# Optimization experiments

Measured on AMD Instinct MI355X. Metric: run time of the kernel, lower is better.

## Reference

```python
import jax, jax.numpy as jnp
import numpy as np

T, B, OBS, ACT = 512, 256, 64, 8
H, C = 1024, 512  # h_size, cell_size


def setup_inputs() -> dict:
    key = jax.random.key(0)
    ks = jax.random.split(key, 12)
    u = lambda k, shape, s: jax.random.uniform(k, shape, jnp.float32, -s, s)
    inp = {
        "xs": jax.random.normal(ks[0], (T, B, OBS), jnp.float32),
        "h0": jnp.zeros((B, C), jnp.float32),
        "c0": jnp.zeros((B, C), jnp.float32),
        "h_masks": (jax.random.uniform(ks[1], (T, B, 1)) < 0.05).astype(jnp.float32),
        # input_layer (kaiming-ish uniform fan-in init)
        "W_in": u(ks[2], (H, OBS), 1.0 / np.sqrt(OBS)),
        "b_in": jnp.zeros((H,), jnp.float32),
        # LSTMCell params, PyTorch layout: gates order (i, f, g, o), [4C, in]
        "W_ih": u(ks[3], (4 * C, H), 1.0 / np.sqrt(C)),
        "b_ih": u(ks[4], (4 * C,), 1.0 / np.sqrt(C)),
        "W_hh": u(ks[5], (4 * C, C), 1.0 / np.sqrt(C)),
        "b_hh": u(ks[6], (4 * C,), 1.0 / np.sqrt(C)),
        # mean_layer with mini_weight_init: U(-0.003, 0.003), zero bias
        "W_mean": u(ks[7], (ACT, C), 0.003),
        "b_mean": jnp.zeros((ACT,), jnp.float32),
        "log_std_param": jax.random.normal(ks[8], (ACT,)) * 1e-10 - 1.0,
    }
    return inp


def reference(xs, h0, c0, h_masks, W_in, b_in, W_ih, b_ih, W_hh, b_hh,
              W_mean, b_mean, log_std_param):
    # xs: [T, B, OBS] -> relu embedding [T, B, H]
    x_emb = jax.nn.relu(jnp.einsum('tbo,ho->tbh', xs, W_in) + b_in)
    # Precompute the input-to-gates GEMM for all timesteps at once: [T, B, 4C]
    gx = jnp.einsum('tbh,gh->tbg', x_emb, W_ih) + b_ih

    cell = W_hh.shape[1]

    def step(carry, inp):
        h, c = carry
        g_x, mask = inp                      # g_x: [B,4C], mask: [B,1]
        keep = 1.0 - mask
        h = h * keep
        c = c * keep
        gates = g_x + h @ W_hh.T + b_hh      # [B, 4C]
        i, f, g, o = jnp.split(gates, 4, axis=-1)
        c = jax.nn.sigmoid(f) * c + jax.nn.sigmoid(i) * jnp.tanh(g)
        h = jax.nn.sigmoid(o) * jnp.tanh(c)
        return (h, c), h

    (h_T, c_T), hiddens = jax.lax.scan(step, (h0, c0), (gx, h_masks))
    # hiddens: [T, B, C]
    means = jnp.tanh(jnp.einsum('tbc,ac->tba', hiddens, W_mean) + b_mean)
    log_std = jnp.broadcast_to(log_std_param, means.shape)
    return means, log_std, h_T, c_T
```

## Files before the change

kernel.cpp:

```cpp
#include <hip/hip_runtime.h>
#include <cstdint>
#include <cstddef>

typedef unsigned short ushort_t;
typedef unsigned int uint_t;
typedef __attribute__((ext_vector_type(8))) __bf16 bf16x8;
typedef __attribute__((ext_vector_type(4))) float f32x4;
typedef __attribute__((ext_vector_type(2))) unsigned int u32x2;

static constexpr int T_STEPS = 512;
static constexpr int BATCH   = 256;
static constexpr int OBS_D   = 64;
static constexpr int ACT_D   = 8;
static constexpr int HID_D   = 1024;
static constexpr int CELL_D  = 512;
static constexpr int GATE_D  = 4 * CELL_D;
static constexpr int SCAN_BLOCKS = 256;

__device__ __forceinline__ float bf2f(ushort_t s) {
    uint_t u = ((uint_t)s) << 16;
    float f;
    __builtin_memcpy(&f, &u, 4);
    return f;
}
__device__ __forceinline__ ushort_t f2bf(float x) {
    uint_t u;
    __builtin_memcpy(&u, &x, 4);
    u += 0x7fffu + ((u >> 16) & 1u);
    return (ushort_t)(u >> 16);
}

__device__ __forceinline__ float sigmoid_fast(float x) {
    return __builtin_amdgcn_rcpf(1.f + __expf(-x));
}
__device__ __forceinline__ float tanh_fast(float x) {
    const float e = __expf(-2.f * fabsf(x));
    const float r = (1.f - e) * __builtin_amdgcn_rcpf(1.f + e);
    return copysignf(r, x);
}

__global__ __launch_bounds__(256)
void cvt_f32_bf16(const float* __restrict__ in, ushort_t* __restrict__ out)
{
    const size_t i = ((size_t)blockIdx.x * 256 + threadIdx.x) * 8;
    const float4 v0 = *(const float4*)(in + i);
    const float4 v1 = *(const float4*)(in + i + 4);
    uint4 p;
    p.x = (uint_t)f2bf(v0.x) | ((uint_t)f2bf(v0.y) << 16);
    p.y = (uint_t)f2bf(v0.z) | ((uint_t)f2bf(v0.w) << 16);
    p.z = (uint_t)f2bf(v1.x) | ((uint_t)f2bf(v1.y) << 16);
    p.w = (uint_t)f2bf(v1.z) | ((uint_t)f2bf(v1.w) << 16);
    *(uint4*)(out + i) = p;
}

__global__ __launch_bounds__(256)
void permute_gate_rows(const float* __restrict__ W, ushort_t* __restrict__ Wp, int K)
{
    const int P = blockIdx.x;
    const int c = P >> 2, g = P & 3;
    const float* src = W + (size_t)(g * CELL_D + c) * K;
    ushort_t* dst = Wp + (size_t)P * K;
    for (int k = threadIdx.x; k < K; k += 256) dst[k] = f2bf(src[k]);
}

__global__ __launch_bounds__(256)
void permute_whh_rows(const float* __restrict__ W, ushort_t* __restrict__ Wp, int K)
{
    const int P = blockIdx.x;
    const int blk = P >> 6, rl = P & 63;
    const int t = rl >> 4, qq = (rl >> 2) & 3, r = rl & 3;
    const float* src = W + (size_t)(r * CELL_D + blk * 16 + t * 4 + qq) * K;
    ushort_t* dst = Wp + (size_t)P * K;
    for (int k = threadIdx.x; k < K; k += 256) dst[k] = f2bf(src[k]);
}

__global__ __launch_bounds__(256)
void permute_bias(const float* __restrict__ b, float* __restrict__ bp)
{
    const int P = blockIdx.x * 256 + threadIdx.x;
    bp[P] = b[(P & 3) * CELL_D + (P >> 2)];
}

template<int OUT_MODE>
__global__ __launch_bounds__(256)
void gemm_mfma_nt(const ushort_t* __restrict__ A, const ushort_t* __restrict__ B,
                  const float* __restrict__ bias, void* __restrict__ out_,
                  int N, int K)
{
    __shared__ __align__(16) ushort_t As[128 * 32];
    __shared__ __align__(16) ushort_t Bs[128 * 32];
    const int tid  = threadIdx.x;
    const int lane = tid & 63;
    const int wid  = tid >> 6;
    const int wr   = (wid >> 1) * 64;
    const int wc   = (wid & 1) * 64;
    const int m0 = blockIdx.y * 128;
    const int n0 = blockIdx.x * 128;

    const int srow = tid >> 2;
    const int sv   = tid & 3;
    const int fr   = lane & 15;
    const int fo   = lane >> 4;

    f32x4 acc[4][4];
#pragma unroll
    for (int i = 0; i < 4; ++i)
#pragma unroll
        for (int j = 0; j < 4; ++j) acc[i][j] = (f32x4){0.f, 0.f, 0.f, 0.f};

    const ushort_t* Apt = A + (size_t)(m0 + srow) * K + sv * 8;
    const ushort_t* Bpt = B + (size_t)(n0 + srow) * K + sv * 8;
    uint4* As4 = (uint4*)As;
    uint4* Bs4 = (uint4*)Bs;
    const bf16x8* Af = (const bf16x8*)As;
    const bf16x8* Bf = (const bf16x8*)Bs;

    for (int k0 = 0; k0 < K; k0 += 32) {
        const uint4 a0 = *(const uint4*)(Apt + k0);
        const uint4 a1 = *(const uint4*)(Apt + (size_t)64 * K + k0);
        const uint4 b0 = *(const uint4*)(Bpt + k0);
        const uint4 b1 = *(const uint4*)(Bpt + (size_t)64 * K + k0);
        __syncthreads();
        As4[srow * 4 + sv]        = a0;
        As4[(64 + srow) * 4 + sv] = a1;
        Bs4[srow * 4 + sv]        = b0;
        Bs4[(64 + srow) * 4 + sv] = b1;
        __syncthreads();

        bf16x8 av[4], bv[4];
#pragma unroll
        for (int m = 0; m < 4; ++m) av[m] = Af[(wr + m * 16 + fr) * 4 + fo];
#pragma unroll
        for (int n = 0; n < 4; ++n) bv[n] = Bf[(wc + n * 16 + fr) * 4 + fo];
#pragma unroll
        for (int m = 0; m < 4; ++m)
#pragma unroll
            for (int n = 0; n < 4; ++n)
                acc[m][n] = __builtin_amdgcn_mfma_f32_16x16x32_bf16(
                    av[m], bv[n], acc[m][n], 0, 0, 0);
    }

#pragma unroll
    for (int n = 0; n < 4; ++n) {
        const int col = n0 + wc + n * 16 + fr;
        const float bvv = bias[col];
#pragma unroll
        for (int m = 0; m < 4; ++m) {
            const int row0 = m0 + wr + m * 16 + fo * 4;
#pragma unroll
            for (int r = 0; r < 4; ++r) {
                const float v = acc[m][n][r] + bvv;
                if constexpr (OUT_MODE == 1)
                    ((ushort_t*)out_)[(size_t)(row0 + r) * N + col] = f2bf(fmaxf(v, 0.f));
                else if constexpr (OUT_MODE == 2)
                    ((ushort_t*)out_)[(size_t)(row0 + r) * N + col] = f2bf(v);
                else
                    ((float*)out_)[(size_t)(row0 + r) * N + col] = v;
            }
        }
    }
}

__device__ __forceinline__ void loadq(uint4 (&d0)[4], uint4 (&d1)[4],
                                      const ushort_t* hr0, const ushort_t* hr1,
                                      int base)
{
#pragma unroll
    for (int j = 0; j < 4; ++j) {
        d0[j] = *(const uint4*)(hr0 + (base + j) * 32);
        d1[j] = *(const uint4*)(hr1 + (base + j) * 32);
    }
}

__device__ __forceinline__ void compq(const uint4 (&d0)[4], const uint4 (&d1)[4],
                                      const char* wsrow, int q16, int xmask,
                                      int base, f32x4& acc0, f32x4& acc1)
{
#pragma unroll
    for (int j = 0; j < 4; ++j) {
        bf16x8 hv0, hv1;
        __builtin_memcpy(&hv0, &d0[j], 16);
        __builtin_memcpy(&hv1, &d1[j], 16);
        const int koff = ((base + j) * 64 + q16) ^ xmask;
        const bf16x8 av = *(const bf16x8*)(wsrow + koff);
        acc0 = __builtin_amdgcn_mfma_f32_16x16x32_bf16(av, hv0, acc0, 0, 0, 0);
        acc1 = __builtin_amdgcn_mfma_f32_16x16x32_bf16(av, hv1, acc1, 0, 0, 0);
    }
}

__global__ __launch_bounds__(256)
void lstm_scan(const ushort_t* __restrict__ gx_p,
               const ushort_t* __restrict__ Whh_p,
               const float* __restrict__ b_hh,
               const float* __restrict__ masks_c,
               const ushort_t* h_init,
               float* __restrict__ c_state,
               ushort_t* hid,
               float* __restrict__ hT_f32,
               int Tc, int is_last,
               uint_t* __restrict__ bar)
{
    __shared__ __align__(16) ushort_t Ws[64 * 512];

    const int tid  = threadIdx.x;
    const int lane = tid & 63;
    const int w    = tid >> 6;
    const int q    = lane >> 4;
    const int s    = lane & 15;
    const int x    = blockIdx.x & 7;
    const int j    = blockIdx.x >> 3;
    const int xmask = (s & 7) << 4;
    const int q16  = q * 16;
    const int cell = j * 16 + w * 4 + q;

    for (int idx = tid; idx < 64 * 64; idx += 256) {
        const int row = idx >> 6;
        const int c16 = idx & 63;
        const uint4 v = *(const uint4*)(Whh_p + (size_t)(j * 64 + row) * CELL_D + c16 * 8);
        *(uint4*)((char*)Ws + row * 1024 + ((c16 * 16) ^ ((row & 7) << 4))) = v;
    }

    const int b0 = x * 32 + s;
    const int b1 = b0 + 16;

    float creg0 = c_state[(size_t)b0 * CELL_D + cell];
    float creg1 = c_state[(size_t)b1 * CELL_D + cell];
    float bh[4];
#pragma unroll
    for (int r = 0; r < 4; ++r) bh[r] = b_hh[r * CELL_D + cell];

    float mv0, mv1;
    uint2 gxv[2];
    auto prefetch_step = [&](int TL) {
        const ushort_t* g0 = gx_p + ((size_t)TL * BATCH + b0) * GATE_D + cell * 4;
        gxv[0] = *(const uint2*)g0;
        gxv[1] = *(const uint2*)(g0 + (size_t)16 * GATE_D);
        mv0 = masks_c[(size_t)TL * BATCH + b0];
        mv1 = masks_c[(size_t)TL * BATCH + b1];
    };

    const char* wsrow = (const char*)Ws + (w * 16 + s) * 1024;
    __syncthreads();

    for (int tl = 0; tl < Tc; ++tl) {
        const ushort_t* hp = (tl == 0) ? h_init
                                       : hid + (size_t)(tl - 1) * BATCH * CELL_D;
        const ushort_t* hr0 = hp + (size_t)b0 * CELL_D + q * 8;
        const ushort_t* hr1 = hp + (size_t)b1 * CELL_D + q * 8;

        uint64_t ready = 0;
        const uint_t tgt_in = (uint_t)tl;
        auto waitg = [&](int g) {
            const uint64_t need = 0xFFull << (g * 8);
            if ((ready & need) != need) {
                const uint_t* fp = bar + x * 32 + (lane & 31);
                for (;;) {
                    uint_t v;
                    asm volatile("global_load_dword %0, %1, off sc0 sc1\n\t"
                                 "s_waitcnt vmcnt(0)"
                                 : "=v"(v) : "v"(fp) : "memory");
                    ready = __ballot((int)(v >= tgt_in)) & 0xFFFFFFFFull;
                    if ((ready & need) == need) break;
                    __builtin_amdgcn_s_sleep(1);
                }
            }
            asm volatile("" ::: "memory");
        };

        f32x4 acc0 = (f32x4){0.f, 0.f, 0.f, 0.f};
        f32x4 acc1 = (f32x4){0.f, 0.f, 0.f, 0.f};

        uint4 A0[4], A1[4], B0[4], B1[4];
        if (tl) waitg(0);
        loadq(A0, A1, hr0, hr1, 0);
        prefetch_step(tl);
        if (tl) waitg(1);
        loadq(B0, B1, hr0, hr1, 4);
        compq(A0, A1, wsrow, q16, xmask, 0, acc0, acc1);
        if (tl) waitg(2);
        loadq(A0, A1, hr0, hr1, 8);
        compq(B0, B1, wsrow, q16, xmask, 4, acc0, acc1);
        if (tl) waitg(3);
        loadq(B0, B1, hr0, hr1, 12);
        compq(A0, A1, wsrow, q16, xmask, 8, acc0, acc1);
        compq(B0, B1, wsrow, q16, xmask, 12, acc0, acc1);

        const float keep0 = (mv0 > 0.5f) ? 0.f : 1.f;
        const float keep1 = (mv1 > 0.5f) ? 0.f : 1.f;
        const ushort_t* gp0 = (const ushort_t*)&gxv[0];
        const ushort_t* gp1 = (const ushort_t*)&gxv[1];

        const float gi0 = fmaf(acc0[0], keep0, bf2f(gp0[0]) + bh[0]);
        const float gf0 = fmaf(acc0[1], keep0, bf2f(gp0[1]) + bh[1]);
        const float gg0 = fmaf(acc0[2], keep0, bf2f(gp0[2]) + bh[2]);
        const float go0 = fmaf(acc0[3], keep0, bf2f(gp0[3]) + bh[3]);
        const float cn0 = sigmoid_fast(gf0) * (creg0 * keep0)
                        + sigmoid_fast(gi0) * tanh_fast(gg0);
        const float hn0 = sigmoid_fast(go0) * tanh_fast(cn0);
        creg0 = cn0;

        const float gi1 = fmaf(acc1[0], keep1, bf2f(gp1[0]) + bh[0]);
        const float gf1 = fmaf(acc1[1], keep1, bf2f(gp1[1]) + bh[1]);
        const float gg1 = fmaf(acc1[2], keep1, bf2f(gp1[2]) + bh[2]);
        const float go1 = fmaf(acc1[3], keep1, bf2f(gp1[3]) + bh[3]);
        const float cn1 = sigmoid_fast(gf1) * (creg1 * keep1)
                        + sigmoid_fast(gi1) * tanh_fast(gg1);
        const float hn1 = sigmoid_fast(go1) * tanh_fast(cn1);
        creg1 = cn1;

        const uint_t hv01 = (uint_t)f2bf(hn0) | ((uint_t)f2bf(hn1) << 16);
        const uint_t vA = (uint_t)__shfl((int)hv01, s + 16);
        const uint_t vB = (uint_t)__shfl((int)hv01, s + 32);
        const uint_t vC = (uint_t)__shfl((int)hv01, s + 48);
        if (q == 0) {
            u32x2 r0, r1;
            r0[0] = (hv01 & 0xFFFFu) | (vA << 16);
            r0[1] = (vB & 0xFFFFu) | (vC << 16);
            r1[0] = (hv01 >> 16) | (vA & 0xFFFF0000u);
            r1[1] = (vB >> 16) | (vC & 0xFFFF0000u);
            ushort_t* d0 = hid + (size_t)tl * BATCH * CELL_D
                         + (size_t)b0 * CELL_D + j * 16 + w * 4;
            ushort_t* d1 = hid + (size_t)tl * BATCH * CELL_D
                         + (size_t)b1 * CELL_D + j * 16 + w * 4;
            asm volatile("global_store_dwordx2 %0, %1, off sc0 sc1"
                         :: "v"(d0), "v"(r0) : "memory");
            asm volatile("global_store_dwordx2 %0, %1, off sc0 sc1"
                         :: "v"(d1), "v"(r1) : "memory");
        }
        if (is_last && tl == Tc - 1) {
            hT_f32[(size_t)b0 * CELL_D + cell] = hn0;
            hT_f32[(size_t)b1 * CELL_D + cell] = hn1;
        }

        if (tl == Tc - 1) break;

        asm volatile("s_waitcnt vmcnt(0)" ::: "memory");
        __builtin_amdgcn_s_barrier();
        if (tid == 0) {
            const uint_t tgt = (uint_t)(tl + 1);
            asm volatile("global_store_dword %0, %1, off sc0 sc1"
                         :: "v"(bar + x * 32 + j), "v"(tgt) : "memory");
        }
    }

    c_state[(size_t)b0 * CELL_D + cell] = creg0;
    c_state[(size_t)b1 * CELL_D + cell] = creg1;
}

__global__ __launch_bounds__(256)
void mean_head(const ushort_t* __restrict__ hiddens, const float* __restrict__ W_mean,
               const float* __restrict__ b_mean, const float* __restrict__ log_std,
               float* __restrict__ means_out, float* __restrict__ logstd_out)
{
    __shared__ float Wm[8][516];
    const int tid = threadIdx.x;
#pragma unroll
    for (int i = 0; i < 16; ++i) {
        int idx = i * 256 + tid;
        Wm[idx >> 9][idx & 511] = W_mean[idx];
    }
    __syncthreads();
    const int r = tid >> 3, a = tid & 7;
    const size_t m = (size_t)blockIdx.x * 32 + r;
    const ushort_t* hp = hiddens + m * CELL_D;
    float acc = 0.f;
#pragma unroll 2
    for (int k8 = 0; k8 < 64; ++k8) {
        const uint4 v = *(const uint4*)(hp + k8 * 8);
        const ushort_t* pv = (const ushort_t*)&v;
        const float* wv = &Wm[a][k8 * 8];
#pragma unroll
        for (int e = 0; e < 8; ++e) acc = fmaf(bf2f(pv[e]), wv[e], acc);
    }
    means_out[m * ACT_D + a]  = tanhf(acc + b_mean[a]);
    logstd_out[m * ACT_D + a] = log_std[a];
}

extern "C" void kernel_launch(void* const* d_in, const int* in_sizes, int n_in,
                              void* d_out, int out_size, void* d_ws, size_t ws_size,
                              hipStream_t stream)
{
    const float* xs     = (const float*)d_in[0];
    const float* h0     = (const float*)d_in[1];
    const float* c0     = (const float*)d_in[2];
    const float* masks  = (const float*)d_in[3];
    const float* W_in   = (const float*)d_in[4];
    const float* b_in   = (const float*)d_in[5];
    const float* W_ih   = (const float*)d_in[6];
    const float* b_ih   = (const float*)d_in[7];
    const float* W_hh   = (const float*)d_in[8];
    const float* b_hh   = (const float*)d_in[9];
    const float* W_mean = (const float*)d_in[10];
    const float* b_mean = (const float*)d_in[11];
    const float* lstd   = (const float*)d_in[12];

    const int M = T_STEPS * BATCH;
    const size_t stateB = (size_t)BATCH * CELL_D * sizeof(float);

    const size_t szWhh  = (size_t)GATE_D * CELL_D * 2;
    const size_t szWih  = (size_t)GATE_D * HID_D * 2;
    const size_t szWin  = (size_t)HID_D * OBS_D * 2;
    const size_t szH0b  = (size_t)BATCH * CELL_D * 2;
    const size_t szBih  = (size_t)GATE_D * 4;
    const size_t szBar  = 1024;
    const size_t fixed  = szWhh + szWih + szWin + szH0b + szBih + szBar + stateB;

    const size_t per_tc = (size_t)BATCH * GATE_D * 2
                        + (size_t)BATCH * CELL_D * 2
                        + (size_t)BATCH * HID_D * 2
                        + (size_t)BATCH * OBS_D * 2;
    int Tc = T_STEPS;
    while (Tc > 2 && fixed + per_tc * (size_t)Tc > ws_size) Tc >>= 1;

    char* p = (char*)d_ws;
    ushort_t* Whh_p = (ushort_t*)p;              p += szWhh;
    ushort_t* Wih_p = (ushort_t*)p;              p += szWih;
    ushort_t* Win_b = (ushort_t*)p;              p += szWin;
    ushort_t* h0b   = (ushort_t*)p;              p += szH0b;
    float*    bihp  = (float*)p;                 p += szBih;
    uint_t*   bar   = (uint_t*)p;                p += szBar;
    float*    c_state = (float*)p;               p += stateB;
    ushort_t* gx_p  = (ushort_t*)p;              p += (size_t)Tc * BATCH * GATE_D * 2;
    ushort_t* hid   = (ushort_t*)p;              p += (size_t)Tc * BATCH * CELL_D * 2;
    ushort_t* E     = (ushort_t*)p;              p += (size_t)Tc * BATCH * HID_D * 2;
    ushort_t* xs_b  = (ushort_t*)p;

    float* means_out  = (float*)d_out;
    float* logstd_out = means_out + (size_t)M * ACT_D;
    float* hT_out     = logstd_out + (size_t)M * ACT_D;
    float* cT_out     = hT_out + (size_t)BATCH * CELL_D;

    permute_whh_rows<<<GATE_D, 256, 0, stream>>>(W_hh, Whh_p, CELL_D);
    permute_gate_rows<<<GATE_D, 256, 0, stream>>>(W_ih, Wih_p, HID_D);
    cvt_f32_bf16<<<(HID_D * OBS_D) / 2048, 256, 0, stream>>>(W_in, Win_b);
    cvt_f32_bf16<<<(BATCH * CELL_D) / 2048, 256, 0, stream>>>(h0, h0b);
    permute_bias<<<GATE_D / 256, 256, 0, stream>>>(b_ih, bihp);
    hipMemcpyAsync(c_state, c0, stateB, hipMemcpyDeviceToDevice, stream);

    const int chunks = T_STEPS / Tc;
    for (int ci = 0; ci < chunks; ++ci) {
        const int t0 = ci * Tc;
        const int Mc = Tc * BATCH;

        cvt_f32_bf16<<<(Mc * OBS_D) / 2048, 256, 0, stream>>>(
            xs + (size_t)t0 * BATCH * OBS_D, xs_b);

        gemm_mfma_nt<1><<<dim3(HID_D / 128, Mc / 128), 256, 0, stream>>>(
            xs_b, Win_b, b_in, E, HID_D, OBS_D);

        gemm_mfma_nt<2><<<dim3(GATE_D / 128, Mc / 128), 256, 0, stream>>>(
            E, Wih_p, bihp, gx_p, GATE_D, HID_D);

        hipMemsetAsync(bar, 0, 1024, stream);
        const ushort_t* h_init = (ci == 0) ? h0b
                               : hid + (size_t)(Tc - 1) * BATCH * CELL_D;
        lstm_scan<<<SCAN_BLOCKS, 256, 0, stream>>>(
            gx_p, Whh_p, b_hh, masks + (size_t)t0 * BATCH, h_init,
            c_state, hid, hT_out, Tc, (ci == chunks - 1) ? 1 : 0, bar);

        mean_head<<<Mc / 32, 256, 0, stream>>>(
            hid, W_mean, b_mean, lstd,
            means_out + (size_t)t0 * BATCH * ACT_D,
            logstd_out + (size_t)t0 * BATCH * ACT_D);
    }

    hipMemcpyAsync(cT_out, c_state, stateB, hipMemcpyDeviceToDevice, stream);
}
```

Baseline: 3.714 ms.

## Split scan block batch halves across twice as many wavefronts

The recurrent LSTM scan kernel now launches 512 threads per block instead of 256. Each wave handles one 16-row batch half instead of both, which halves the per-thread h loads, MFMAs and gate math on the serial critical path. The W_hh tile in shared memory is now shared by 8 waves rather than 4. The cost is more waves taking part in the per-step block barrier and higher per-block resource use. Each step's latency is expected to fall from the added parallelism within a block.

```diff
diff --git a/kernel.cpp b/kernel.cpp
--- a/kernel.cpp
+++ b/kernel.cpp
@@ -161,34 +161,27 @@
     }
 }
 
-__device__ __forceinline__ void loadq(uint4 (&d0)[4], uint4 (&d1)[4],
-                                      const ushort_t* hr0, const ushort_t* hr1,
-                                      int base)
+__device__ __forceinline__ void loadq1(uint4 (&d)[4], const ushort_t* hr, int base)
+{
+#pragma unroll
+    for (int j = 0; j < 4; ++j) d[j] = *(const uint4*)(hr + (base + j) * 32);
+}
+
+__device__ __forceinline__ void compq1(const uint4 (&d)[4],
+                                       const char* wsrow, int q16, int xmask,
+                                       int base, f32x4& acc)
 {
 #pragma unroll
     for (int j = 0; j < 4; ++j) {
-        d0[j] = *(const uint4*)(hr0 + (base + j) * 32);
-        d1[j] = *(const uint4*)(hr1 + (base + j) * 32);
-    }
-}
-
-__device__ __forceinline__ void compq(const uint4 (&d0)[4], const uint4 (&d1)[4],
-                                      const char* wsrow, int q16, int xmask,
-                                      int base, f32x4& acc0, f32x4& acc1)
-{
-#pragma unroll
-    for (int j = 0; j < 4; ++j) {
-        bf16x8 hv0, hv1;
-        __builtin_memcpy(&hv0, &d0[j], 16);
-        __builtin_memcpy(&hv1, &d1[j], 16);
+        bf16x8 hv;
+        __builtin_memcpy(&hv, &d[j], 16);
         const int koff = ((base + j) * 64 + q16) ^ xmask;
         const bf16x8 av = *(const bf16x8*)(wsrow + koff);
-        acc0 = __builtin_amdgcn_mfma_f32_16x16x32_bf16(av, hv0, acc0, 0, 0, 0);
-        acc1 = __builtin_amdgcn_mfma_f32_16x16x32_bf16(av, hv1, acc1, 0, 0, 0);
-    }
-}
-
-__global__ __launch_bounds__(256)
+        acc = __builtin_amdgcn_mfma_f32_16x16x32_bf16(av, hv, acc, 0, 0, 0);
+    }
+}
+
+__global__ __launch_bounds__(512)
 void lstm_scan(const ushort_t* __restrict__ gx_p,
                const ushort_t* __restrict__ Whh_p,
                const float* __restrict__ b_hh,
@@ -204,7 +197,9 @@
 
     const int tid  = threadIdx.x;
     const int lane = tid & 63;
-    const int w    = tid >> 6;
+    const int w8   = tid >> 6;
+    const int w    = w8 & 3;
+    const int nfl  = w8 >> 2;
     const int q    = lane >> 4;
     const int s    = lane & 15;
     const int x    = blockIdx.x & 7;
@@ -213,30 +208,25 @@
     const int q16  = q * 16;
     const int cell = j * 16 + w * 4 + q;
 
-    for (int idx = tid; idx < 64 * 64; idx += 256) {
+    for (int idx = tid; idx < 64 * 64; idx += 512) {
         const int row = idx >> 6;
         const int c16 = idx & 63;
         const uint4 v = *(const uint4*)(Whh_p + (size_t)(j * 64 + row) * CELL_D + c16 * 8);
         *(uint4*)((char*)Ws + row * 1024 + ((c16 * 16) ^ ((row & 7) << 4))) = v;
     }
 
-    const int b0 = x * 32 + s;
-    const int b1 = b0 + 16;
-
-    float creg0 = c_state[(size_t)b0 * CELL_D + cell];
-    float creg1 = c_state[(size_t)b1 * CELL_D + cell];
+    const int b = x * 32 + nfl * 16 + s;
+
+    float creg = c_state[(size_t)b * CELL_D + cell];
     float bh[4];
 #pragma unroll
     for (int r = 0; r < 4; ++r) bh[r] = b_hh[r * CELL_D + cell];
 
-    float mv0, mv1;
-    uint2 gxv[2];
+    float mv;
+    uint2 gxv;
     auto prefetch_step = [&](int TL) {
-        const ushort_t* g0 = gx_p + ((size_t)TL * BATCH + b0) * GATE_D + cell * 4;
-        gxv[0] = *(const uint2*)g0;
-        gxv[1] = *(const uint2*)(g0 + (size_t)16 * GATE_D);
-        mv0 = masks_c[(size_t)TL * BATCH + b0];
-        mv1 = masks_c[(size_t)TL * BATCH + b1];
+        gxv = *(const uint2*)(gx_p + ((size_t)TL * BATCH + b) * GATE_D + cell * 4);
+        mv  = masks_c[(size_t)TL * BATCH + b];
     };
 
     const char* wsrow = (const char*)Ws + (w * 16 + s) * 1024;
@@ -245,8 +235,7 @@
     for (int tl = 0; tl < Tc; ++tl) {
         const ushort_t* hp = (tl == 0) ? h_init
                                        : hid + (size_t)(tl - 1) * BATCH * CELL_D;
-        const ushort_t* hr0 = hp + (size_t)b0 * CELL_D + q * 8;
-        const ushort_t* hr1 = hp + (size_t)b1 * CELL_D + q * 8;
+        const ushort_t* hr = hp + (size_t)b * CELL_D + q * 8;
 
         uint64_t ready = 0;
         const uint_t tgt_in = (uint_t)tl;
@@ -267,70 +256,49 @@
             asm volatile("" ::: "memory");
         };
 
-        f32x4 acc0 = (f32x4){0.f, 0.f, 0.f, 0.f};
-        f32x4 acc1 = (f32x4){0.f, 0.f, 0.f, 0.f};
-
-        uint4 A0[4], A1[4], B0[4], B1[4];
+        f32x4 acc = (f32x4){0.f, 0.f, 0.f, 0.f};
+
+        uint4 A[4], B[4];
         if (tl) waitg(0);
-        loadq(A0, A1, hr0, hr1, 0);
+        loadq1(A, hr, 0);
         prefetch_step(tl);
         if (tl) waitg(1);
-        loadq(B0, B1, hr0, hr1, 4);
-        compq(A0, A1, wsrow, q16, xmask, 0, acc0, acc1);
+        loadq1(B, hr, 4);
+        compq1(A, wsrow, q16, xmask, 0, acc);
         if (tl) waitg(2);
-        loadq(A0, A1, hr0, hr1, 8);
-        compq(B0, B1, wsrow, q16, xmask, 4, acc0, acc1);
+        loadq1(A, hr, 8);
+        compq1(B, wsrow, q16, xmask, 4, acc);
         if (tl) waitg(3);
-        loadq(B0, B1, hr0, hr1, 12);
-        compq(A0, A1, wsrow, q16, xmask, 8, acc0, acc1);
-        compq(B0, B1, wsrow, q16, xmask, 12, acc0, acc1);
-
-        const float keep0 = (mv0 > 0.5f) ? 0.f : 1.f;
-        const float keep1 = (mv1 > 0.5f) ? 0.f : 1.f;
-        const ushort_t* gp0 = (const ushort_t*)&gxv[0];
-        const ushort_t* gp1 = (const ushort_t*)&gxv[1];
-
-        const float gi0 = fmaf(acc0[0], keep0, bf2f(gp0[0]) + bh[0]);
-        const float gf0 = fmaf(acc0[1], keep0, bf2f(gp0[1]) + bh[1]);
-        const float gg0 = fmaf(acc0[2], keep0, bf2f(gp0[2]) + bh[2]);
-        const float go0 = fmaf(acc0[3], keep0, bf2f(gp0[3]) + bh[3]);
-        const float cn0 = sigmoid_fast(gf0) * (creg0 * keep0)
-                        + sigmoid_fast(gi0) * tanh_fast(gg0);
-        const float hn0 = sigmoid_fast(go0) * tanh_fast(cn0);
-        creg0 = cn0;
-
-        const float gi1 = fmaf(acc1[0], keep1, bf2f(gp1[0]) + bh[0]);
-        const float gf1 = fmaf(acc1[1], keep1, bf2f(gp1[1]) + bh[1]);
-        const float gg1 = fmaf(acc1[2], keep1, bf2f(gp1[2]) + bh[2]);
-        const float go1 = fmaf(acc1[3], keep1, bf2f(gp1[3]) + bh[3]);
-        const float cn1 = sigmoid_fast(gf1) * (creg1 * keep1)
-                        + sigmoid_fast(gi1) * tanh_fast(gg1);
-        const float hn1 = sigmoid_fast(go1) * tanh_fast(cn1);
-        creg1 = cn1;
-
-        const uint_t hv01 = (uint_t)f2bf(hn0) | ((uint_t)f2bf(hn1) << 16);
-        const uint_t vA = (uint_t)__shfl((int)hv01, s + 16);
-        const uint_t vB = (uint_t)__shfl((int)hv01, s + 32);
-        const uint_t vC = (uint_t)__shfl((int)hv01, s + 48);
+        loadq1(B, hr, 12);
+        compq1(A, wsrow, q16, xmask, 8, acc);
+        compq1(B, wsrow, q16, xmask, 12, acc);
+
+        const float keep = (mv > 0.5f) ? 0.f : 1.f;
+        const ushort_t* gp = (const ushort_t*)&gxv;
+        const float gi = fmaf(acc[0], keep, bf2f(gp[0]) + bh[0]);
+        const float gf = fmaf(acc[1], keep, bf2f(gp[1]) + bh[1]);
+        const float gg = fmaf(acc[2], keep, bf2f(gp[2]) + bh[2]);
+        const float go = fmaf(acc[3], keep, bf2f(gp[3]) + bh[3]);
+        const float cn = sigmoid_fast(gf) * (creg * keep)
+                       + sigmoid_fast(gi) * tanh_fast(gg);
+        const float hn = sigmoid_fast(go) * tanh_fast(cn);
+        creg = cn;
+
+        const uint_t hv = (uint_t)f2bf(hn);
+        const uint_t vA = (uint_t)__shfl((int)hv, s + 16);
+        const uint_t vB = (uint_t)__shfl((int)hv, s + 32);
+        const uint_t vC = (uint_t)__shfl((int)hv, s + 48);
         if (q == 0) {
-            u32x2 r0, r1;
-            r0[0] = (hv01 & 0xFFFFu) | (vA << 16);
-            r0[1] = (vB & 0xFFFFu) | (vC << 16);
-            r1[0] = (hv01 >> 16) | (vA & 0xFFFF0000u);
-            r1[1] = (vB >> 16) | (vC & 0xFFFF0000u);
+            u32x2 r0;
+            r0[0] = hv | (vA << 16);
+            r0[1] = vB | (vC << 16);
             ushort_t* d0 = hid + (size_t)tl * BATCH * CELL_D
-                         + (size_t)b0 * CELL_D + j * 16 + w * 4;
-            ushort_t* d1 = hid + (size_t)tl * BATCH * CELL_D
-                         + (size_t)b1 * CELL_D + j * 16 + w * 4;
+                         + (size_t)b * CELL_D + j * 16 + w * 4;
             asm volatile("global_store_dwordx2 %0, %1, off sc0 sc1"
                          :: "v"(d0), "v"(r0) : "memory");
-            asm volatile("global_store_dwordx2 %0, %1, off sc0 sc1"
-                         :: "v"(d1), "v"(r1) : "memory");
         }
-        if (is_last && tl == Tc - 1) {
-            hT_f32[(size_t)b0 * CELL_D + cell] = hn0;
-            hT_f32[(size_t)b1 * CELL_D + cell] = hn1;
-        }
+        if (is_last && tl == Tc - 1)
+            hT_f32[(size_t)b * CELL_D + cell] = hn;
 
         if (tl == Tc - 1) break;
 
@@ -343,8 +311,7 @@
         }
     }
 
-    c_state[(size_t)b0 * CELL_D + cell] = creg0;
-    c_state[(size_t)b1 * CELL_D + cell] = creg1;
+    c_state[(size_t)b * CELL_D + cell] = creg;
 }
 
 __global__ __launch_bounds__(256)
@@ -454,7 +421,7 @@
         hipMemsetAsync(bar, 0, 1024, stream);
         const ushort_t* h_init = (ci == 0) ? h0b
                                : hid + (size_t)(Tc - 1) * BATCH * CELL_D;
-        lstm_scan<<<SCAN_BLOCKS, 256, 0, stream>>>(
+        lstm_scan<<<SCAN_BLOCKS, 512, 0, stream>>>(
             gx_p, Whh_p, b_hh, masks + (size_t)t0 * BATCH, h_init,
             c_state, hid, hT_out, Tc, (ci == chunks - 1) ? 1 : 0, bar);
 
```

After: 3.726 ms. Within noise of the previous version (+0.3%).
